# Optimization experiments

Hardware: AMD Instinct MI355X
Metric: run time of the kernel (lower is better)

## Reference

```python
import jax, jax.numpy as jnp
import numpy as np

RSQRT2 = 2 ** (-0.5)
B, S, D_IN = 2, 4096, 1024
H, D_HEAD = 8, 64            # num_heads, attention_dim (per-head qk and v dim)
QK_DIM = H * D_HEAD          # 512
V_DIM = H * D_HEAD           # 512
OUT_DIM = D_IN               # 1024 (output_dim defaults to input_dim)
LN_EPS = 1e-5


def setup_inputs() -> dict:
    key = jax.random.key(0)
    ks = jax.random.split(key, 8)
    def lecun(k, fan_in, shape):
        return jax.random.normal(k, shape, dtype=jnp.float32) * (1.0 / np.sqrt(fan_in))
    return {
        "x": jax.random.normal(ks[0], (B, S, D_IN), dtype=jnp.float32),
        # weights stored [in, out] (transposed torch Linear layout)
        "W_qk": lecun(ks[1], D_IN, (D_IN, 2 * QK_DIM)),
        "b_qk": jnp.zeros((2 * QK_DIM,), jnp.float32),
        "W_v": lecun(ks[2], D_IN, (D_IN, V_DIM)),
        "b_v": jnp.zeros((V_DIM,), jnp.float32),
        "W_out": lecun(ks[3], V_DIM, (V_DIM, OUT_DIM)),
        "b_out": jnp.zeros((OUT_DIM,), jnp.float32),
        "ln_gamma": jnp.ones((OUT_DIM,), jnp.float32),
        "ln_beta": jnp.zeros((OUT_DIM,), jnp.float32),
    }


def _layernorm(y, gamma, beta):
    mu = jnp.mean(y, axis=-1, keepdims=True)
    var = jnp.mean(jnp.square(y - mu), axis=-1, keepdims=True)
    return (y - mu) * jax.lax.rsqrt(var + LN_EPS) * gamma + beta


def reference(x, W_qk, b_qk, W_v, b_v, W_out, b_out, ln_gamma, ln_beta):
    b, s, _ = x.shape
    scale = D_HEAD ** (-0.5)
    qk = x @ W_qk + b_qk                          # [b, s, 2*h*d]
    qk = qk.reshape(b, s, H, D_HEAD, 2)           # c (q/k) is fastest axis
    q, k = qk[..., 0], qk[..., 1]                 # [b, s, h, d]
    v = (x @ W_v + b_v).reshape(b, s, H, D_HEAD)  # [b, s, h, d]
    # manual multi-head attention, full O(s^2) score matrix (as in source)
    sim = jnp.einsum("bihd,bjhd->bhij", q, k) * scale
    attn = jax.nn.softmax(sim, axis=-1)           # [b, h, i, j]
    o = jnp.einsum("bhij,bjhd->bihd", attn, v)    # [b, s, h, d]
    o = o.reshape(b, s, V_DIM)                    # 'b h s d -> b s (h d)'
    y = _layernorm(o @ W_out + b_out, ln_gamma, ln_beta)
    return (y + x) * RSQRT2
```

## Files before the change

### kernel.cpp

```cpp
#include <hip/hip_runtime.h>
#include <stdint.h>

typedef short bf16x8 __attribute__((ext_vector_type(8)));
typedef float f32x4 __attribute__((ext_vector_type(4)));
typedef unsigned short ushort_t;

#define RSQRT2_F 0.70710678118654752440f
#define QSCALE_F 0.18033688011114382f

__device__ __forceinline__ ushort_t f2bf(float f) {
  union { float f; uint32_t u; } c; c.f = f;
  uint32_t u = c.u;
  uint32_t r = (u + 0x7fffu + ((u >> 16) & 1u)) >> 16;
  return (ushort_t)r;
}
__device__ __forceinline__ float bf2f(ushort_t u) {
  union { uint32_t u; float f; } c; c.u = ((uint32_t)u) << 16;
  return c.f;
}
__device__ __forceinline__ uint32_t fbits(float f) {
  union { float f; uint32_t u; } c; c.f = f; return c.u;
}

__device__ __forceinline__ void gload_lds16(const void* g, void* l) {
  __builtin_amdgcn_global_load_lds(
      (const __attribute__((address_space(1))) void*)g,
      (__attribute__((address_space(3))) void*)l, 16, 0, 0);
}

__global__ __launch_bounds__(256) void k_cvt_x(const float* __restrict__ x,
                                               ushort_t* __restrict__ xb) {
  int i = (blockIdx.x * 256 + threadIdx.x) * 4;
  float4 f = *(const float4*)(x + i);
  ushort4 o;
  o.x = f2bf(f.x); o.y = f2bf(f.y); o.z = f2bf(f.z); o.w = f2bf(f.w);
  *(ushort4*)(xb + i) = o;
}

__global__ __launch_bounds__(256) void k_build_wqkv(const float* __restrict__ Wqk,
                                                    const float* __restrict__ bqk,
                                                    const float* __restrict__ Wv,
                                                    const float* __restrict__ bv,
                                                    ushort_t* __restrict__ Wt,
                                                    float* __restrict__ biasAll) {
  int k = blockIdx.x * 256 + threadIdx.x;
  int n = blockIdx.y;
  float w, bb;
  if (n < 512)       { w = Wqk[(size_t)k * 1024 + 2 * n] * QSCALE_F;     bb = bqk[2 * n] * QSCALE_F; }
  else if (n < 1024) { w = Wqk[(size_t)k * 1024 + 2 * (n - 512) + 1];    bb = bqk[2 * (n - 512) + 1]; }
  else               { w = Wv[(size_t)k * 512 + (n - 1024)];             bb = bv[n - 1024]; }
  Wt[(size_t)n * 1024 + k] = f2bf(w);
  if (k == 0) biasAll[n] = bb;
}

__global__ __launch_bounds__(256) void k_build_wout(const float* __restrict__ Wout,
                                                    ushort_t* __restrict__ Wt) {
  int k = blockIdx.x * 256 + threadIdx.x;
  int n = blockIdx.y;
  Wt[(size_t)n * 512 + k] = f2bf(Wout[(size_t)k * 1024 + n]);
}

template <int MODE>
__global__ __launch_bounds__(256) void k_gemm_bt(
    const ushort_t* __restrict__ A, const ushort_t* __restrict__ Bt,
    const float* __restrict__ bias,
    ushort_t* __restrict__ out0, ushort_t* __restrict__ out1, ushort_t* __restrict__ out2,
    int M, int N, int K) {
  __shared__ __align__(16) ushort_t As[2][4][128][8];
  __shared__ __align__(16) ushort_t Bs[2][4][128][8];
  const int t = threadIdx.x;
  const int lane = t & 63;
  const int wave = t >> 6;

  const int nby = N >> 7;
  const int nwg = gridDim.x;
  const int xcd = blockIdx.x & 7, pos = blockIdx.x >> 3;
  const int swz = xcd * (nwg >> 3) + pos;
  const int bx = swz / nby, by = swz % nby;
  const int m0 = bx * 128, n0 = by * 128;

  const int wm = (wave >> 1) * 64, wn = (wave & 1) * 64;
  const int lg = lane >> 4, lr = lane & 15;

  const int srow = t & 127, sg = t >> 7;
  const ushort_t* gA = A + (size_t)(m0 + srow) * K + sg * 8;
  const ushort_t* gB = Bt + (size_t)(n0 + srow) * K + sg * 8;

  f32x4 acc[4][4] = {};

#define GEMM_STAGE(k0, bsel)                                   \
  do {                                                         \
    gload_lds16(gA + (k0), &As[bsel][sg][srow][0]);            \
    gload_lds16(gA + (k0) + 16, &As[bsel][sg + 2][srow][0]);   \
    gload_lds16(gB + (k0), &Bs[bsel][sg][srow][0]);            \
    gload_lds16(gB + (k0) + 16, &Bs[bsel][sg + 2][srow][0]);   \
  } while (0)

  GEMM_STAGE(0, 0);
  __syncthreads();
  int buf = 0;
  for (int k0 = 0; k0 < K; k0 += 32) {
    if (k0 + 32 < K) GEMM_STAGE(k0 + 32, buf ^ 1);
    bf16x8 af[4], bfr[4];
#pragma unroll
    for (int mi = 0; mi < 4; mi++) af[mi] = *(const bf16x8*)&As[buf][lg][wm + mi * 16 + lr][0];
#pragma unroll
    for (int ni = 0; ni < 4; ni++) bfr[ni] = *(const bf16x8*)&Bs[buf][lg][wn + ni * 16 + lr][0];
#pragma unroll
    for (int mi = 0; mi < 4; mi++)
#pragma unroll
      for (int ni = 0; ni < 4; ni++)
        acc[mi][ni] = __builtin_amdgcn_mfma_f32_16x16x32_bf16(af[mi], bfr[ni], acc[mi][ni], 0, 0, 0);
    __syncthreads();
    buf ^= 1;
  }
#undef GEMM_STAGE

#pragma unroll
  for (int mi = 0; mi < 4; mi++) {
    int rowb = m0 + wm + mi * 16 + (lane >> 4) * 4;
#pragma unroll
    for (int ni = 0; ni < 4; ni++) {
      int col = n0 + wn + ni * 16 + lr;
      float bc = bias[col];
#pragma unroll
      for (int reg = 0; reg < 4; reg++) {
        int row = rowb + reg;
        float v = acc[mi][ni][reg] + bc;
        if (MODE == 0) {
          if (col < 512) {
            out0[(size_t)row * 512 + col] = f2bf(v);
          } else if (col < 1024) {
            out1[(size_t)row * 512 + (col - 512)] = f2bf(v);
          } else {
            int hd = col - 1024;
            int bb = row >> 12, s = row & 4095;
            out2[((size_t)(bb << 9) + hd) * 4096 + s] = f2bf(v);
          }
        } else {
          out0[(size_t)row * 1024 + col] = f2bf(v);
        }
      }
    }
  }
}

__global__ __launch_bounds__(256, 4) void k_attn(const ushort_t* __restrict__ Qb,
                                                 const ushort_t* __restrict__ Kb,
                                                 const ushort_t* __restrict__ Vt,
                                                 ushort_t* __restrict__ Ob) {
  __shared__ __align__(16) ushort_t Ks[2][8][64][8];
  __shared__ __align__(16) ushort_t Vs[2][8][64][8];
  __shared__ __align__(16) ushort_t Pl[4][1024];
  const int S = 4096;
  const int t = threadIdx.x, lane = t & 63, wave = t >> 6;
  const int lg = lane >> 4, lr = lane & 15;

  const int bid = blockIdx.x;
  const int xcd = bid & 7, idx = bid >> 3;
  const int bh = (xcd << 1) | (idx >> 6);
  const int qb = idx & 63;
  const int b = bh >> 3, h = bh & 7;
  const int qbase = qb * 64 + wave * 16;

  const ushort_t* qp = Qb + ((size_t)(b * S + qbase + lr)) * 512 + h * 64 + lg * 8;
  const bf16x8 qf0 = *(const bf16x8*)qp;
  const bf16x8 qf1 = *(const bf16x8*)(qp + 32);

  const int cj = t & 63, cg = t >> 6;
  const ushort_t* gK = Kb + ((size_t)b * S + cj) * 512 + h * 64 + cg * 8;
  const ushort_t* gV = Vt + ((size_t)bh * 64 + cj) * 4096 + cg * 8;

  char* Pbase = (char*)&Pl[wave][0];

  const bf16x8 vones = {(short)0x3F80, (short)0x3F80, (short)0x3F80, (short)0x3F80,
                        (short)0x3F80, (short)0x3F80, (short)0x3F80, (short)0x3F80};

  f32x4 of[4] = {};
  f32x4 of_sum = {};
  float m_run = -1e30f;

#define ATTN_STAGE(kv0, bsel)                                         \
  do {                                                                \
    gload_lds16(gK + (size_t)(kv0) * 512, &Ks[bsel][cg][cj][0]);      \
    gload_lds16(gK + (size_t)(kv0) * 512 + 32, &Ks[bsel][cg + 4][cj][0]); \
    gload_lds16(gV + (kv0), &Vs[bsel][cg][cj][0]);                    \
    gload_lds16(gV + (kv0) + 32, &Vs[bsel][cg + 4][cj][0]);           \
  } while (0)

  ATTN_STAGE(0, 0);
  __syncthreads();
  int buf = 0;

  for (int kv0 = 0; kv0 < S; kv0 += 64) {
    if (kv0 + 64 < S) ATTN_STAGE(kv0 + 64, buf ^ 1);

    f32x4 sf[4];
#pragma unroll
    for (int nt = 0; nt < 4; nt++) {
      bf16x8 kf0 = *(const bf16x8*)&Ks[buf][lg][nt * 16 + lr][0];
      bf16x8 kf1 = *(const bf16x8*)&Ks[buf][4 + lg][nt * 16 + lr][0];
      f32x4 z = {};
      z = __builtin_amdgcn_mfma_f32_16x16x32_bf16(kf0, qf0, z, 0, 0, 0);
      sf[nt] = __builtin_amdgcn_mfma_f32_16x16x32_bf16(kf1, qf1, z, 0, 0, 0);
    }

    float pmax = sf[0][0];
#pragma unroll
    for (int nt = 0; nt < 4; nt++)
#pragma unroll
      for (int r = 0; r < 4; r++) pmax = fmaxf(pmax, sf[nt][r]);
    pmax = fmaxf(pmax, __shfl_xor(pmax, 16, 64));
    pmax = fmaxf(pmax, __shfl_xor(pmax, 32, 64));

    if (__any(pmax > m_run + 11.0f)) {
      float mnew = fmaxf(m_run, pmax);
      float scl = __builtin_amdgcn_exp2f(m_run - mnew);
      m_run = mnew;
      float sclr[4];
#pragma unroll
      for (int r = 0; r < 4; r++) sclr[r] = __shfl(scl, lg * 4 + r, 64);
#pragma unroll
      for (int dt = 0; dt < 4; dt++)
#pragma unroll
        for (int r = 0; r < 4; r++) of[dt][r] *= sclr[r];
#pragma unroll
      for (int r = 0; r < 4; r++) of_sum[r] *= sclr[r];
    }

#pragma unroll
    for (int nt = 0; nt < 4; nt++) {
      float p0 = __builtin_amdgcn_exp2f(sf[nt][0] - m_run);
      float p1 = __builtin_amdgcn_exp2f(sf[nt][1] - m_run);
      float p2 = __builtin_amdgcn_exp2f(sf[nt][2] - m_run);
      float p3 = __builtin_amdgcn_exp2f(sf[nt][3] - m_run);
      uint32_t w0 = (fbits(p0) >> 16) | (fbits(p1) & 0xffff0000u);
      uint32_t w1 = (fbits(p2) >> 16) | (fbits(p3) & 0xffff0000u);
      int off = (lr * 128 + nt * 32 + lg * 8) ^ ((lr & 7) << 4);
      *(uint2*)(Pbase + off) = make_uint2(w0, w1);
    }

    bf16x8 pf[2];
#pragma unroll
    for (int kc = 0; kc < 2; kc++) {
      int off = (lr * 128 + kc * 64 + lg * 16) ^ ((lr & 7) << 4);
      pf[kc] = *(const bf16x8*)(Pbase + off);
    }

#pragma unroll
    for (int dt = 0; dt < 4; dt++) {
      bf16x8 vf0 = *(const bf16x8*)&Vs[buf][lg][dt * 16 + lr][0];
      bf16x8 vf1 = *(const bf16x8*)&Vs[buf][4 + lg][dt * 16 + lr][0];
      of[dt] = __builtin_amdgcn_mfma_f32_16x16x32_bf16(pf[0], vf0, of[dt], 0, 0, 0);
      of[dt] = __builtin_amdgcn_mfma_f32_16x16x32_bf16(pf[1], vf1, of[dt], 0, 0, 0);
    }
    of_sum = __builtin_amdgcn_mfma_f32_16x16x32_bf16(pf[0], vones, of_sum, 0, 0, 0);
    of_sum = __builtin_amdgcn_mfma_f32_16x16x32_bf16(pf[1], vones, of_sum, 0, 0, 0);

    __syncthreads();
    buf ^= 1;
  }
#undef ATTN_STAGE

  float inv[4];
#pragma unroll
  for (int r = 0; r < 4; r++) inv[r] = 1.0f / of_sum[r];
#pragma unroll
  for (int dt = 0; dt < 4; dt++)
#pragma unroll
    for (int r = 0; r < 4; r++) {
      int q = qbase + lg * 4 + r;
      Ob[((size_t)b * S + q) * 512 + h * 64 + dt * 16 + lr] = f2bf(of[dt][r] * inv[r]);
    }
}

__global__ __launch_bounds__(256) void k_ln(const ushort_t* __restrict__ ypre,
                                            const float* __restrict__ x,
                                            const float* __restrict__ gamma,
                                            const float* __restrict__ beta,
                                            float* __restrict__ out) {
  __shared__ float red[8];
  const int row = blockIdx.x, t = threadIdx.x;
  const ushort_t* yr = ypre + (size_t)row * 1024;
  ushort4 u = *(const ushort4*)(yr + t * 4);
  float v0 = bf2f(u.x), v1 = bf2f(u.y), v2 = bf2f(u.z), v3 = bf2f(u.w);
  float s = v0 + v1 + v2 + v3;
  float sq = v0 * v0 + v1 * v1 + v2 * v2 + v3 * v3;
#pragma unroll
  for (int m = 32; m; m >>= 1) { s += __shfl_xor(s, m, 64); sq += __shfl_xor(sq, m, 64); }
  if ((t & 63) == 0) { red[t >> 6] = s; red[4 + (t >> 6)] = sq; }
  __syncthreads();
  s = red[0] + red[1] + red[2] + red[3];
  sq = red[4] + red[5] + red[6] + red[7];
  float mu = s * (1.f / 1024.f);
  float var = sq * (1.f / 1024.f) - mu * mu;
  float inv = rsqrtf(var + 1e-5f);
  int c = t * 4;
  float4 xf = *(const float4*)(x + (size_t)row * 1024 + c);
  float4 o;
  o.x = ((v0 - mu) * inv * gamma[c + 0] + beta[c + 0] + xf.x) * RSQRT2_F;
  o.y = ((v1 - mu) * inv * gamma[c + 1] + beta[c + 1] + xf.y) * RSQRT2_F;
  o.z = ((v2 - mu) * inv * gamma[c + 2] + beta[c + 2] + xf.z) * RSQRT2_F;
  o.w = ((v3 - mu) * inv * gamma[c + 3] + beta[c + 3] + xf.w) * RSQRT2_F;
  *(float4*)(out + (size_t)row * 1024 + c) = o;
}

extern "C" void kernel_launch(void* const* d_in, const int* in_sizes, int n_in,
                              void* d_out, int out_size, void* d_ws, size_t ws_size,
                              hipStream_t stream) {
  (void)in_sizes; (void)n_in; (void)out_size; (void)ws_size;
  const float* x     = (const float*)d_in[0];
  const float* Wqk   = (const float*)d_in[1];
  const float* bqk   = (const float*)d_in[2];
  const float* Wv    = (const float*)d_in[3];
  const float* bv    = (const float*)d_in[4];
  const float* Wout  = (const float*)d_in[5];
  const float* bout  = (const float*)d_in[6];
  const float* gamma = (const float*)d_in[7];
  const float* beta  = (const float*)d_in[8];
  float* out = (float*)d_out;

  char* ws = (char*)d_ws;
  size_t off = 0;
  auto alloc = [&](size_t bytes) {
    off = (off + 255) & ~(size_t)255;
    void* p = ws + off;
    off += bytes;
    return p;
  };
  ushort_t* xb    = (ushort_t*)alloc(8192ull * 1024 * 2);
  ushort_t* Wqkvt = (ushort_t*)alloc(1536ull * 1024 * 2);
  float*    biasA = (float*)   alloc(1536ull * 4);
  ushort_t* Woutt = (ushort_t*)alloc(1024ull * 512 * 2);
  ushort_t* Qb    = (ushort_t*)alloc(8192ull * 512 * 2);
  ushort_t* Kbuf  = (ushort_t*)alloc(8192ull * 512 * 2);
  ushort_t* Vtb   = (ushort_t*)alloc(1024ull * 4096 * 2);
  ushort_t* Ob    = (ushort_t*)alloc(8192ull * 512 * 2);
  ushort_t* ypre  = xb;

  k_cvt_x<<<8192, 256, 0, stream>>>(x, xb);
  k_build_wqkv<<<dim3(4, 1536), 256, 0, stream>>>(Wqk, bqk, Wv, bv, Wqkvt, biasA);
  k_build_wout<<<dim3(2, 1024), 256, 0, stream>>>(Wout, Woutt);
  k_gemm_bt<0><<<768, 256, 0, stream>>>(xb, Wqkvt, biasA, Qb, Kbuf, Vtb, 8192, 1536, 1024);
  k_attn<<<1024, 256, 0, stream>>>(Qb, Kbuf, Vtb, Ob);
  k_gemm_bt<1><<<512, 256, 0, stream>>>(Ob, Woutt, bout, ypre, nullptr, nullptr, 8192, 1024, 512);
  k_ln<<<8192, 256, 0, stream>>>(ypre, x, gamma, beta, out);
}
```

Baseline: 247.2 us.

## Process two query sub-tiles per wave to reuse K/V LDS fragments

Result: no change. 247.2 us (+0.0%).

```diff
diff --git a/kernel.cpp b/kernel.cpp
--- a/kernel.cpp
+++ b/kernel.cpp
@@ -145,40 +145,42 @@
   }
 }
 
-__global__ __launch_bounds__(256, 4) void k_attn(const ushort_t* __restrict__ Qb,
-                                                 const ushort_t* __restrict__ Kb,
-                                                 const ushort_t* __restrict__ Vt,
-                                                 ushort_t* __restrict__ Ob) {
+__global__ __launch_bounds__(256) void k_attn(const ushort_t* __restrict__ Qb,
+                                              const ushort_t* __restrict__ Kb,
+                                              const ushort_t* __restrict__ Vt,
+                                              ushort_t* __restrict__ Ob) {
   __shared__ __align__(16) ushort_t Ks[2][8][64][8];
   __shared__ __align__(16) ushort_t Vs[2][8][64][8];
-  __shared__ __align__(16) ushort_t Pl[4][1024];
+  __shared__ __align__(16) ushort_t Pl[4][2][1024];
   const int S = 4096;
   const int t = threadIdx.x, lane = t & 63, wave = t >> 6;
   const int lg = lane >> 4, lr = lane & 15;
 
   const int bid = blockIdx.x;
   const int xcd = bid & 7, idx = bid >> 3;
-  const int bh = (xcd << 1) | (idx >> 6);
-  const int qb = idx & 63;
+  const int bh = (xcd << 1) | (idx >> 5);
+  const int qb = idx & 31;
   const int b = bh >> 3, h = bh & 7;
-  const int qbase = qb * 64 + wave * 16;
-
-  const ushort_t* qp = Qb + ((size_t)(b * S + qbase + lr)) * 512 + h * 64 + lg * 8;
-  const bf16x8 qf0 = *(const bf16x8*)qp;
-  const bf16x8 qf1 = *(const bf16x8*)(qp + 32);
+  const int qbase = qb * 128 + wave * 32;
+
+  bf16x8 qf[2][2];
+#pragma unroll
+  for (int su = 0; su < 2; su++) {
+    const ushort_t* qp = Qb + ((size_t)(b * S + qbase + su * 16 + lr)) * 512 + h * 64 + lg * 8;
+    qf[su][0] = *(const bf16x8*)qp;
+    qf[su][1] = *(const bf16x8*)(qp + 32);
+  }
 
   const int cj = t & 63, cg = t >> 6;
   const ushort_t* gK = Kb + ((size_t)b * S + cj) * 512 + h * 64 + cg * 8;
   const ushort_t* gV = Vt + ((size_t)bh * 64 + cj) * 4096 + cg * 8;
 
-  char* Pbase = (char*)&Pl[wave][0];
-
   const bf16x8 vones = {(short)0x3F80, (short)0x3F80, (short)0x3F80, (short)0x3F80,
                         (short)0x3F80, (short)0x3F80, (short)0x3F80, (short)0x3F80};
 
-  f32x4 of[4] = {};
-  f32x4 of_sum = {};
-  float m_run = -1e30f;
+  f32x4 of[2][4] = {};
+  f32x4 of_sum[2] = {};
+  float m_run[2] = {-1e30f, -1e30f};
 
 #define ATTN_STAGE(kv0, bsel)                                         \
   do {                                                                \
@@ -195,83 +197,99 @@
   for (int kv0 = 0; kv0 < S; kv0 += 64) {
     if (kv0 + 64 < S) ATTN_STAGE(kv0 + 64, buf ^ 1);
 
-    f32x4 sf[4];
+    f32x4 sf[2][4];
 #pragma unroll
     for (int nt = 0; nt < 4; nt++) {
       bf16x8 kf0 = *(const bf16x8*)&Ks[buf][lg][nt * 16 + lr][0];
       bf16x8 kf1 = *(const bf16x8*)&Ks[buf][4 + lg][nt * 16 + lr][0];
-      f32x4 z = {};
-      z = __builtin_amdgcn_mfma_f32_16x16x32_bf16(kf0, qf0, z, 0, 0, 0);
-      sf[nt] = __builtin_amdgcn_mfma_f32_16x16x32_bf16(kf1, qf1, z, 0, 0, 0);
-    }
-
-    float pmax = sf[0][0];
-#pragma unroll
-    for (int nt = 0; nt < 4; nt++)
-#pragma unroll
-      for (int r = 0; r < 4; r++) pmax = fmaxf(pmax, sf[nt][r]);
-    pmax = fmaxf(pmax, __shfl_xor(pmax, 16, 64));
-    pmax = fmaxf(pmax, __shfl_xor(pmax, 32, 64));
-
-    if (__any(pmax > m_run + 11.0f)) {
-      float mnew = fmaxf(m_run, pmax);
-      float scl = __builtin_amdgcn_exp2f(m_run - mnew);
-      m_run = mnew;
-      float sclr[4];
-#pragma unroll
-      for (int r = 0; r < 4; r++) sclr[r] = __shfl(scl, lg * 4 + r, 64);
-#pragma unroll
-      for (int dt = 0; dt < 4; dt++)
-#pragma unroll
-        for (int r = 0; r < 4; r++) of[dt][r] *= sclr[r];
-#pragma unroll
-      for (int r = 0; r < 4; r++) of_sum[r] *= sclr[r];
-    }
-
-#pragma unroll
-    for (int nt = 0; nt < 4; nt++) {
-      float p0 = __builtin_amdgcn_exp2f(sf[nt][0] - m_run);
-      float p1 = __builtin_amdgcn_exp2f(sf[nt][1] - m_run);
-      float p2 = __builtin_amdgcn_exp2f(sf[nt][2] - m_run);
-      float p3 = __builtin_amdgcn_exp2f(sf[nt][3] - m_run);
-      uint32_t w0 = (fbits(p0) >> 16) | (fbits(p1) & 0xffff0000u);
-      uint32_t w1 = (fbits(p2) >> 16) | (fbits(p3) & 0xffff0000u);
-      int off = (lr * 128 + nt * 32 + lg * 8) ^ ((lr & 7) << 4);
-      *(uint2*)(Pbase + off) = make_uint2(w0, w1);
-    }
-
-    bf16x8 pf[2];
-#pragma unroll
-    for (int kc = 0; kc < 2; kc++) {
-      int off = (lr * 128 + kc * 64 + lg * 16) ^ ((lr & 7) << 4);
-      pf[kc] = *(const bf16x8*)(Pbase + off);
+#pragma unroll
+      for (int su = 0; su < 2; su++) {
+        f32x4 z = {};
+        z = __builtin_amdgcn_mfma_f32_16x16x32_bf16(kf0, qf[su][0], z, 0, 0, 0);
+        sf[su][nt] = __builtin_amdgcn_mfma_f32_16x16x32_bf16(kf1, qf[su][1], z, 0, 0, 0);
+      }
+    }
+
+    bf16x8 pf[2][2];
+#pragma unroll
+    for (int su = 0; su < 2; su++) {
+      float pmax = sf[su][0][0];
+#pragma unroll
+      for (int nt = 0; nt < 4; nt++)
+#pragma unroll
+        for (int r = 0; r < 4; r++) pmax = fmaxf(pmax, sf[su][nt][r]);
+      pmax = fmaxf(pmax, __shfl_xor(pmax, 16, 64));
+      pmax = fmaxf(pmax, __shfl_xor(pmax, 32, 64));
+
+      if (__any(pmax > m_run[su] + 11.0f)) {
+        float mnew = fmaxf(m_run[su], pmax);
+        float scl = __builtin_amdgcn_exp2f(m_run[su] - mnew);
+        m_run[su] = mnew;
+        float sclr[4];
+#pragma unroll
+        for (int r = 0; r < 4; r++) sclr[r] = __shfl(scl, lg * 4 + r, 64);
+#pragma unroll
+        for (int dt = 0; dt < 4; dt++)
+#pragma unroll
+          for (int r = 0; r < 4; r++) of[su][dt][r] *= sclr[r];
+#pragma unroll
+        for (int r = 0; r < 4; r++) of_sum[su][r] *= sclr[r];
+      }
+
+      char* Pb = (char*)&Pl[wave][su][0];
+#pragma unroll
+      for (int nt = 0; nt < 4; nt++) {
+        float p0 = __builtin_amdgcn_exp2f(sf[su][nt][0] - m_run[su]);
+        float p1 = __builtin_amdgcn_exp2f(sf[su][nt][1] - m_run[su]);
+        float p2 = __builtin_amdgcn_exp2f(sf[su][nt][2] - m_run[su]);
+        float p3 = __builtin_amdgcn_exp2f(sf[su][nt][3] - m_run[su]);
+        uint32_t w0 = (fbits(p0) >> 16) | (fbits(p1) & 0xffff0000u);
+        uint32_t w1 = (fbits(p2) >> 16) | (fbits(p3) & 0xffff0000u);
+        int off = (lr * 128 + nt * 32 + lg * 8) ^ ((lr & 7) << 4);
+        *(uint2*)(Pb + off) = make_uint2(w0, w1);
+      }
+
+#pragma unroll
+      for (int kc = 0; kc < 2; kc++) {
+        int off = (lr * 128 + kc * 64 + lg * 16) ^ ((lr & 7) << 4);
+        pf[su][kc] = *(const bf16x8*)(Pb + off);
+      }
     }
 
 #pragma unroll
     for (int dt = 0; dt < 4; dt++) {
       bf16x8 vf0 = *(const bf16x8*)&Vs[buf][lg][dt * 16 + lr][0];
       bf16x8 vf1 = *(const bf16x8*)&Vs[buf][4 + lg][dt * 16 + lr][0];
-      of[dt] = __builtin_amdgcn_mfma_f32_16x16x32_bf16(pf[0], vf0, of[dt], 0, 0, 0);
-      of[dt] = __builtin_amdgcn_mfma_f32_16x16x32_bf16(pf[1], vf1, of[dt], 0, 0, 0);
-    }
-    of_sum = __builtin_amdgcn_mfma_f32_16x16x32_bf16(pf[0], vones, of_sum, 0, 0, 0);
-    of_sum = __builtin_amdgcn_mfma_f32_16x16x32_bf16(pf[1], vones, of_sum, 0, 0, 0);
+#pragma unroll
+      for (int su = 0; su < 2; su++) {
+        of[su][dt] = __builtin_amdgcn_mfma_f32_16x16x32_bf16(pf[su][0], vf0, of[su][dt], 0, 0, 0);
+        of[su][dt] = __builtin_amdgcn_mfma_f32_16x16x32_bf16(pf[su][1], vf1, of[su][dt], 0, 0, 0);
+      }
+    }
+#pragma unroll
+    for (int su = 0; su < 2; su++) {
+      of_sum[su] = __builtin_amdgcn_mfma_f32_16x16x32_bf16(pf[su][0], vones, of_sum[su], 0, 0, 0);
+      of_sum[su] = __builtin_amdgcn_mfma_f32_16x16x32_bf16(pf[su][1], vones, of_sum[su], 0, 0, 0);
+    }
 
     __syncthreads();
     buf ^= 1;
   }
 #undef ATTN_STAGE
 
-  float inv[4];
-#pragma unroll
-  for (int r = 0; r < 4; r++) inv[r] = 1.0f / of_sum[r];
-#pragma unroll
-  for (int dt = 0; dt < 4; dt++)
-#pragma unroll
-    for (int r = 0; r < 4; r++) {
-      int q = qbase + lg * 4 + r;
-      Ob[((size_t)b * S + q) * 512 + h * 64 + dt * 16 + lr] = f2bf(of[dt][r] * inv[r]);
-    }
+#pragma unroll
+  for (int su = 0; su < 2; su++) {
+    float inv[4];
+#pragma unroll
+    for (int r = 0; r < 4; r++) inv[r] = 1.0f / of_sum[su][r];
+#pragma unroll
+    for (int dt = 0; dt < 4; dt++)
+#pragma unroll
+      for (int r = 0; r < 4; r++) {
+        int q = qbase + su * 16 + lg * 4 + r;
+        Ob[((size_t)b * S + q) * 512 + h * 64 + dt * 16 + lr] = f2bf(of[su][dt][r] * inv[r]);
+      }
+  }
 }
 
 __global__ __launch_bounds__(256) void k_ln(const ushort_t* __restrict__ ypre,
@@ -342,7 +360,7 @@
   k_build_wqkv<<<dim3(4, 1536), 256, 0, stream>>>(Wqk, bqk, Wv, bv, Wqkvt, biasA);
   k_build_wout<<<dim3(2, 1024), 256, 0, stream>>>(Wout, Woutt);
   k_gemm_bt<0><<<768, 256, 0, stream>>>(xb, Wqkvt, biasA, Qb, Kbuf, Vtb, 8192, 1536, 1024);
-  k_attn<<<1024, 256, 0, stream>>>(Qb, Kbuf, Vtb, Ob);
+  k_attn<<<512, 256, 0, stream>>>(Qb, Kbuf, Vtb, Ob);
   k_gemm_bt<1><<<512, 256, 0, stream>>>(Ob, Woutt, bout, ypre, nullptr, nullptr, 8192, 1024, 512);
   k_ln<<<8192, 256, 0, stream>>>(ypre, x, gamma, beta, out);
 }
```
